# Kernel optimization log

Measured on AMD Instinct MI355X. Metric: run time of the kernel, lower is better.

## Reference

```python
import jax, jax.numpy as jnp
import numpy as np

SPATIAL_SHAPES = ((100, 167), (50, 84), (25, 42), (13, 21))
NUM_HEADS = 8
NUM_LEVELS = 4
NUM_POINTS = 4
EMBED_DIM = 256
LV = sum(h * w for h, w in SPATIAL_SHAPES)  # 22223


def bilinear_sample(img, grid):
    """torch.F.grid_sample(mode='bilinear', padding_mode='zeros', align_corners=False).
    img: (B, D, H, W); grid: (B, Lq, P, 2) with xy in [-1, 1]. Returns (B, D, Lq, P)."""
    B, D, H, W = img.shape
    x = (grid[..., 0] + 1.0) * 0.5 * W - 0.5  # (B, Lq, P)
    y = (grid[..., 1] + 1.0) * 0.5 * H - 0.5
    x0 = jnp.floor(x)
    y0 = jnp.floor(y)
    wx1 = x - x0
    wy1 = y - y0
    wx0 = 1.0 - wx1
    wy0 = 1.0 - wy1

    def gather(ix, iy):
        valid = ((ix >= 0) & (ix <= W - 1) & (iy >= 0) & (iy <= H - 1)).astype(img.dtype)
        ixc = jnp.clip(ix, 0, W - 1).astype(jnp.int32)
        iyc = jnp.clip(iy, 0, H - 1).astype(jnp.int32)

        def g(img_b, ixb, iyb, vb):
            return img_b[:, iyb, ixb] * vb[None]  # (D, Lq, P)

        return jax.vmap(g)(img, ixc, iyc, valid)  # (B, D, Lq, P)

    v00 = gather(x0, y0)
    v01 = gather(x0 + 1, y0)
    v10 = gather(x0, y0 + 1)
    v11 = gather(x0 + 1, y0 + 1)
    w00 = (wy0 * wx0)[:, None]
    w01 = (wy0 * wx1)[:, None]
    w10 = (wy1 * wx0)[:, None]
    w11 = (wy1 * wx1)[:, None]
    return v00 * w00 + v01 * w01 + v10 * w10 + v11 * w11


def deform_attn(query, ref_points, value, W_off, b_off, W_attn, b_attn, W_val, b_val, W_out, b_out):
    N, Lq, C = query.shape
    D = C // NUM_HEADS
    off = (query @ W_off + b_off).reshape(N, Lq, NUM_HEADS, NUM_LEVELS, NUM_POINTS, 2)
    attn = jax.nn.softmax((query @ W_attn + b_attn).reshape(N, Lq, NUM_HEADS, NUM_LEVELS * NUM_POINTS), axis=-1)
    attn = attn.reshape(N, Lq, NUM_HEADS, NUM_LEVELS, NUM_POINTS)
    ref_cxcy = ref_points[:, :, None, :, None, :2]
    ref_wh = ref_points[:, :, None, :, None, 2:]
    loc = ref_cxcy + off / NUM_POINTS * ref_wh * 0.5
    grids = 2.0 * loc - 1.0  # (N, Lq, nh, L, P, 2)

    v = value @ W_val + b_val  # (N, Lv, C)
    sampled = []
    start = 0
    for lvl, (H, W) in enumerate(SPATIAL_SHAPES):
        v_l = v[:, start:start + H * W]  # (N, HW, C)
        start += H * W
        v_l = v_l.transpose(0, 2, 1).reshape(N * NUM_HEADS, D, H, W)
        g_l = grids[:, :, :, lvl].transpose(0, 2, 1, 3, 4).reshape(N * NUM_HEADS, Lq, NUM_POINTS, 2)
        sampled.append(bilinear_sample(v_l, g_l))  # (N*nh, D, Lq, P)
    sampled = jnp.concatenate(sampled, axis=-1)  # (N*nh, D, Lq, L*P)

    attn_r = attn.transpose(0, 2, 1, 3, 4).reshape(N * NUM_HEADS, 1, Lq, NUM_LEVELS * NUM_POINTS)
    out = (sampled * attn_r).sum(-1)  # (N*nh, D, Lq)
    out = out.reshape(N, C, Lq).transpose(0, 2, 1)
    return out @ W_out + b_out


def setup_inputs() -> dict:
    key = jax.random.key(0)
    ks = jax.random.split(key, 8)
    N, Lq, C = 1, LV, EMBED_DIM
    s = 0.02
    return {
        "query": jax.random.normal(ks[0], (N, Lq, C), jnp.float32),
        "ref_points": jax.random.uniform(ks[1], (N, Lq, NUM_LEVELS, 4), jnp.float32),
        "value": jax.random.normal(ks[2], (N, LV, C), jnp.float32),
        "W_off": jax.random.normal(ks[3], (C, NUM_HEADS * NUM_LEVELS * NUM_POINTS * 2), jnp.float32) * s,
        "b_off": jnp.zeros((NUM_HEADS * NUM_LEVELS * NUM_POINTS * 2,), jnp.float32),
        "W_attn": jax.random.normal(ks[4], (C, NUM_HEADS * NUM_LEVELS * NUM_POINTS), jnp.float32) * s,
        "b_attn": jnp.zeros((NUM_HEADS * NUM_LEVELS * NUM_POINTS,), jnp.float32),
        "W_val": jax.random.normal(ks[5], (C, C), jnp.float32) * s,
        "b_val": jnp.zeros((C,), jnp.float32),
        "W_out": jax.random.normal(ks[6], (C, C), jnp.float32) * s,
        "b_out": jnp.zeros((C,), jnp.float32),
    }


def reference(query, ref_points, value, W_off, b_off, W_attn, b_attn, W_val, b_val, W_out, b_out):
    return deform_attn(query, ref_points, value, W_off, b_off, W_attn, b_attn, W_val, b_val, W_out, b_out)
```

## Files before the change

kernel.cpp:

```cpp
#include <hip/hip_runtime.h>
#include <math.h>

#define LQ 22223
#define NH 8
#define NL 4
#define NP 4
#define CDIM 256

typedef __attribute__((ext_vector_type(8))) short short8;
typedef __attribute__((ext_vector_type(4))) float f32x4;

__device__ __forceinline__ ushort f2bf(float f) {
    union { float f; unsigned u; } c; c.f = f;
    unsigned u = c.u;
    return (ushort)((u + 0x7fffu + ((u >> 16) & 1u)) >> 16);
}
__device__ __forceinline__ float bflo(unsigned u) {
    union { unsigned u; float f; } c; c.u = u << 16; return c.f;
}
__device__ __forceinline__ float bfhi(unsigned u) {
    union { unsigned u; float f; } c; c.u = u & 0xffff0000u; return c.f;
}

__global__ __launch_bounds__(256) void convert_act(
    const float4* __restrict__ q, const float4* __restrict__ v,
    ushort* __restrict__ qb, ushort* __restrict__ vb, int n8each)
{
    int i = blockIdx.x * 256 + threadIdx.x;
    const float4* src; ushort* dst; int j;
    if (i < n8each) { src = q; dst = qb; j = i; }
    else if (i < 2 * n8each) { src = v; dst = vb; j = i - n8each; }
    else return;
    const float4 a = src[2 * j];
    const float4 b = src[2 * j + 1];
    short8 o;
    o[0] = (short)f2bf(a.x); o[1] = (short)f2bf(a.y);
    o[2] = (short)f2bf(a.z); o[3] = (short)f2bf(a.w);
    o[4] = (short)f2bf(b.x); o[5] = (short)f2bf(b.y);
    o[6] = (short)f2bf(b.z); o[7] = (short)f2bf(b.w);
    *reinterpret_cast<short8*>(dst + 8 * j) = o;
}

__global__ __launch_bounds__(256) void convert_wt(
    const float* __restrict__ Wv, const float* __restrict__ Wo,
    const float* __restrict__ Wu, const float* __restrict__ Wa,
    const float* __restrict__ bo, const float* __restrict__ ba,
    ushort* __restrict__ Tv, ushort* __restrict__ Toa,
    ushort* __restrict__ Tu, float* __restrict__ bcat)
{
    int idx = blockIdx.x * 256 + threadIdx.x;
    if (idx >= 229376) {
        int b = idx - 229376;
        if (b < 384) bcat[b] = (b < 256) ? bo[b] : ba[b - 256];
        return;
    }
    const float* W; ushort* T; int N; int local;
    if      (idx < 65536)  { W = Wv; T = Tv;          N = 256; local = idx; }
    else if (idx < 131072) { W = Wo; T = Toa;         N = 256; local = idx - 65536; }
    else if (idx < 196608) { W = Wu; T = Tu;          N = 256; local = idx - 131072; }
    else                   { W = Wa; T = Toa + 65536; N = 128; local = idx - 196608; }
    int k = local & 255;
    int n = local >> 8;
    T[n * 256 + k] = f2bf(W[k * N + n]);
}

template <typename OutT>
__global__ __launch_bounds__(256) void gemm_bf16(
    const ushort* __restrict__ A, const ushort* __restrict__ Bt,
    const float* __restrict__ bias, OutT* __restrict__ C,
    int M, int N)
{
    const int K = 256;
    __shared__ ushort As[64 * 40];
    __shared__ ushort Bs[64 * 40];

    const int tid = threadIdx.x;
    const int w = tid >> 6;
    const int l = tid & 63;
    const int bm = blockIdx.y * 64;
    const int bn = blockIdx.x * 64;

    const int r = tid >> 2;
    const int c = tid & 3;

    const int m_l  = (w << 4) + (l & 15);
    const int koff = (l >> 4) << 3;

    f32x4 acc[4] = {};

    for (int k0 = 0; k0 < K; k0 += 32) {
        short8 av = {0, 0, 0, 0, 0, 0, 0, 0};
        if (bm + r < M)
            av = *reinterpret_cast<const short8*>(A + (size_t)(bm + r) * K + k0 + c * 8);
        const short8 bv = *reinterpret_cast<const short8*>(
            Bt + (size_t)(bn + r) * K + k0 + c * 8);

        __syncthreads();
        *reinterpret_cast<short8*>(&As[r * 40 + c * 8]) = av;
        *reinterpret_cast<short8*>(&Bs[r * 40 + c * 8]) = bv;
        __syncthreads();

        const short8 af = *reinterpret_cast<const short8*>(&As[m_l * 40 + koff]);
        #pragma unroll
        for (int t = 0; t < 4; ++t) {
            const short8 bf = *reinterpret_cast<const short8*>(
                &Bs[(t * 16 + (l & 15)) * 40 + koff]);
            acc[t] = __builtin_amdgcn_mfma_f32_16x16x32_bf16(af, bf, acc[t], 0, 0, 0);
        }
    }

    const int row0 = bm + (w << 4) + ((l >> 4) << 2);
    #pragma unroll
    for (int t = 0; t < 4; ++t) {
        const int col = bn + t * 16 + (l & 15);
        const float bs = bias[col];
        #pragma unroll
        for (int i = 0; i < 4; ++i) {
            const int row = row0 + i;
            if (row < M) {
                const float o = acc[t][i] + bs;
                if constexpr (sizeof(OutT) == 2)
                    C[(size_t)row * N + col] = (OutT)f2bf(o);
                else
                    C[(size_t)row * N + col] = (OutT)o;
            }
        }
    }
}

__global__ __launch_bounds__(256) void softmax16(float* __restrict__ offattn, int rows)
{
    const int r = blockIdx.x * 256 + threadIdx.x;
    if (r >= rows) return;
    const int q = r >> 3;
    const int h = r & 7;
    float4* p = reinterpret_cast<float4*>(offattn + (size_t)q * 384 + 256 + h * 16);
    float v[16];
    #pragma unroll
    for (int i = 0; i < 4; ++i) {
        const float4 f = p[i];
        v[i * 4 + 0] = f.x; v[i * 4 + 1] = f.y; v[i * 4 + 2] = f.z; v[i * 4 + 3] = f.w;
    }
    float m = v[0];
    #pragma unroll
    for (int i = 1; i < 16; ++i) m = fmaxf(m, v[i]);
    float s = 0.f;
    #pragma unroll
    for (int i = 0; i < 16; ++i) { v[i] = expf(v[i] - m); s += v[i]; }
    const float inv = 1.f / s;
    #pragma unroll
    for (int i = 0; i < 4; ++i)
        p[i] = make_float4(v[i * 4 + 0] * inv, v[i * 4 + 1] * inv,
                           v[i * 4 + 2] * inv, v[i * 4 + 3] * inv);
}

__global__ __launch_bounds__(256) void msda_sample(
    const ushort* __restrict__ v, const float* __restrict__ offattn,
    const float* __restrict__ ref, ushort* __restrict__ outp)
{
    __shared__ int4   s_off[1024];
    __shared__ float4 s_wts[1024];

    const int h = blockIdx.x & 7;
    const int qbase = (blockIdx.x >> 3) * 64;
    const int tid = threadIdx.x;

    const int Hs[4] = {100, 50, 25, 13};
    const int Ws[4] = {167, 84, 42, 21};
    const int starts[4] = {0, 16700, 20900, 21950};
    const int h32 = h * 32;

    #pragma unroll
    for (int t2 = 0; t2 < 4; ++t2) {
        const int t = t2 * 256 + tid;
        const int qi = t & 63;
        const int pi = t >> 6;
        const int q = qbase + qi;
        if (q < LQ) {
            const int l = pi >> 2;
            const int W = Ws[l], H = Hs[l];
            const float* refq = ref + (size_t)q * (NL * 4) + l * 4;
            const float cx = refq[0], cy = refq[1], rw = refq[2], rh = refq[3];
            const float* row = offattn + (size_t)q * 384;
            const float ox = row[h32 + pi * 2];
            const float oy = row[h32 + pi * 2 + 1];
            const float wgt = row[256 + h * 16 + pi];

            const float lx = cx + ox * 0.125f * rw;
            const float ly = cy + oy * 0.125f * rh;
            const float x = lx * (float)W - 0.5f;
            const float y = ly * (float)H - 0.5f;

            const float x0f = floorf(x);
            const float y0f = floorf(y);
            const int x0 = (int)x0f, y0 = (int)y0f;
            const float wx1 = x - x0f, wy1 = y - y0f;
            const float wx0 = 1.f - wx1, wy0 = 1.f - wy1;

            const bool xv0 = (x0 >= 0) && (x0 < W);
            const bool xv1 = (x0 + 1 >= 0) && (x0 + 1 < W);
            const bool yv0 = (y0 >= 0) && (y0 < H);
            const bool yv1 = (y0 + 1 >= 0) && (y0 + 1 < H);

            const int x0c = min(max(x0, 0), W - 1);
            const int x1c = min(max(x0 + 1, 0), W - 1);
            const int y0c = min(max(y0, 0), H - 1);
            const int y1c = min(max(y0 + 1, 0), H - 1);

            int4 ob;
            ob.x = ((starts[l] + y0c * W + x0c) << 8) + h32;
            ob.y = ((starts[l] + y0c * W + x1c) << 8) + h32;
            ob.z = ((starts[l] + y1c * W + x0c) << 8) + h32;
            ob.w = ((starts[l] + y1c * W + x1c) << 8) + h32;
            float4 wb;
            wb.x = (xv0 && yv0) ? wgt * wy0 * wx0 : 0.f;
            wb.y = (xv1 && yv0) ? wgt * wy0 * wx1 : 0.f;
            wb.z = (xv0 && yv1) ? wgt * wy1 * wx0 : 0.f;
            wb.w = (xv1 && yv1) ? wgt * wy1 * wx1 : 0.f;
            s_off[t] = ob;
            s_wts[t] = wb;
        }
    }
    __syncthreads();

    const int qi = tid >> 2;
    const int dg = tid & 3;
    const int q = qbase + qi;
    if (q >= LQ) return;
    const int d8 = dg * 8;

    float acc[8] = {};

    int4   o = s_off[qi];
    float4 w = s_wts[qi];
    uint4 a0 = *reinterpret_cast<const uint4*>(v + o.x + d8);
    uint4 a1 = *reinterpret_cast<const uint4*>(v + o.y + d8);
    uint4 a2 = *reinterpret_cast<const uint4*>(v + o.z + d8);
    uint4 a3 = *reinterpret_cast<const uint4*>(v + o.w + d8);

    #pragma unroll
    for (int p = 0; p < 16; ++p) {
        uint4 b0, b1, b2, b3; float4 wn;
        if (p < 15) {
            const int4 on = s_off[(p + 1) * 64 + qi];
            wn = s_wts[(p + 1) * 64 + qi];
            b0 = *reinterpret_cast<const uint4*>(v + on.x + d8);
            b1 = *reinterpret_cast<const uint4*>(v + on.y + d8);
            b2 = *reinterpret_cast<const uint4*>(v + on.z + d8);
            b3 = *reinterpret_cast<const uint4*>(v + on.w + d8);
        }
        const unsigned u0[4] = {a0.x, a0.y, a0.z, a0.w};
        const unsigned u1[4] = {a1.x, a1.y, a1.z, a1.w};
        const unsigned u2[4] = {a2.x, a2.y, a2.z, a2.w};
        const unsigned u3[4] = {a3.x, a3.y, a3.z, a3.w};
        #pragma unroll
        for (int j = 0; j < 4; ++j) {
            acc[2 * j]     += w.x * bflo(u0[j]) + w.y * bflo(u1[j])
                            + w.z * bflo(u2[j]) + w.w * bflo(u3[j]);
            acc[2 * j + 1] += w.x * bfhi(u0[j]) + w.y * bfhi(u1[j])
                            + w.z * bfhi(u2[j]) + w.w * bfhi(u3[j]);
        }
        a0 = b0; a1 = b1; a2 = b2; a3 = b3; w = wn;
    }

    short8 o8;
    #pragma unroll
    for (int j = 0; j < 8; ++j) o8[j] = (short)f2bf(acc[j]);
    *reinterpret_cast<short8*>(outp + (size_t)q * CDIM + h32 + d8) = o8;
}

extern "C" void kernel_launch(void* const* d_in, const int* in_sizes, int n_in,
                              void* d_out, int out_size, void* d_ws, size_t ws_size,
                              hipStream_t stream)
{
    const float* query  = (const float*)d_in[0];
    const float* ref    = (const float*)d_in[1];
    const float* value  = (const float*)d_in[2];
    const float* W_off  = (const float*)d_in[3];
    const float* b_off  = (const float*)d_in[4];
    const float* W_attn = (const float*)d_in[5];
    const float* b_attn = (const float*)d_in[6];
    const float* W_val  = (const float*)d_in[7];
    const float* b_val  = (const float*)d_in[8];
    const float* W_out  = (const float*)d_in[9];
    const float* b_out  = (const float*)d_in[10];
    float* out = (float*)d_out;

    char* p = (char*)d_ws;
    ushort* v_bf    = (ushort*)p; p += (size_t)LQ * CDIM * 2;
    float*  offattn = (float*)p;  p += (size_t)LQ * 384 * 4;
    ushort* q_bf    = (ushort*)p; p += (size_t)LQ * CDIM * 2;
    ushort* val_bf  = (ushort*)p; p += (size_t)LQ * CDIM * 2;
    ushort* Wt_val  = (ushort*)p; p += 65536 * 2;
    ushort* Wt_oa   = (ushort*)p; p += (65536 + 32768) * 2;
    ushort* Wt_out  = (ushort*)p; p += 65536 * 2;
    float*  bcat    = (float*)p;  p += 384 * 4;
    ushort* outp = q_bf;

    const int n8 = LQ * CDIM / 8;
    const int mblk = (LQ + 63) / 64;

    convert_act<<<(2 * n8 + 255) / 256, 256, 0, stream>>>(
        (const float4*)query, (const float4*)value, q_bf, val_bf, n8);
    convert_wt<<<(229376 + 384 + 255) / 256, 256, 0, stream>>>(
        W_val, W_off, W_out, W_attn, b_off, b_attn, Wt_val, Wt_oa, Wt_out, bcat);

    gemm_bf16<ushort><<<dim3(CDIM / 64, mblk), 256, 0, stream>>>(
        val_bf, Wt_val, b_val, v_bf, LQ, CDIM);
    gemm_bf16<float><<<dim3(384 / 64, mblk), 256, 0, stream>>>(
        q_bf, Wt_oa, bcat, offattn, LQ, 384);
    softmax16<<<(LQ * NH + 255) / 256, 256, 0, stream>>>(offattn, LQ * NH);
    const int qg = (LQ + 63) / 64;
    msda_sample<<<qg * 8, 256, 0, stream>>>(v_bf, offattn, ref, outp);
    gemm_bf16<float><<<dim3(CDIM / 64, mblk), 256, 0, stream>>>(
        outp, Wt_out, b_out, out, LQ, CDIM);
}
```

Measured before the change: 235.7 us.

## Fuse fp32-to-bf16 activation conversion into GEMMs and cover full N per block

Drops the separate activation conversion kernel. The GEMMs now read fp32 query/value directly and convert to bf16 while loading tiles. Each GEMM block now covers the full output width (16 or 24 MMA fragments), so every A row tile is read once instead of once per 64-column slab. The sampling kernel's manual software prefetch of the next point is also replaced by a plain loop. The trade-off is fewer, larger blocks (about 348) with more accumulators and shared memory each, which may reduce occupancy, and the GEMMs now read fp32 A at twice the bytes.

```diff
diff --git a/kernel.cpp b/kernel.cpp
--- a/kernel.cpp
+++ b/kernel.cpp
@@ -20,25 +20,6 @@
 }
 __device__ __forceinline__ float bfhi(unsigned u) {
     union { unsigned u; float f; } c; c.u = u & 0xffff0000u; return c.f;
-}
-
-__global__ __launch_bounds__(256) void convert_act(
-    const float4* __restrict__ q, const float4* __restrict__ v,
-    ushort* __restrict__ qb, ushort* __restrict__ vb, int n8each)
-{
-    int i = blockIdx.x * 256 + threadIdx.x;
-    const float4* src; ushort* dst; int j;
-    if (i < n8each) { src = q; dst = qb; j = i; }
-    else if (i < 2 * n8each) { src = v; dst = vb; j = i - n8each; }
-    else return;
-    const float4 a = src[2 * j];
-    const float4 b = src[2 * j + 1];
-    short8 o;
-    o[0] = (short)f2bf(a.x); o[1] = (short)f2bf(a.y);
-    o[2] = (short)f2bf(a.z); o[3] = (short)f2bf(a.w);
-    o[4] = (short)f2bf(b.x); o[5] = (short)f2bf(b.y);
-    o[6] = (short)f2bf(b.z); o[7] = (short)f2bf(b.w);
-    *reinterpret_cast<short8*>(dst + 8 * j) = o;
 }
 
 __global__ __launch_bounds__(256) void convert_wt(
@@ -64,21 +45,20 @@
     T[n * 256 + k] = f2bf(W[k * N + n]);
 }
 
-template <typename OutT>
-__global__ __launch_bounds__(256) void gemm_bf16(
-    const ushort* __restrict__ A, const ushort* __restrict__ Bt,
-    const float* __restrict__ bias, OutT* __restrict__ C,
-    int M, int N)
+template <int NFRAG, typename AT, typename OutT>
+__global__ __launch_bounds__(256) void gemm_full(
+    const AT* __restrict__ A, const ushort* __restrict__ Bt,
+    const float* __restrict__ bias, OutT* __restrict__ C, int M)
 {
     const int K = 256;
+    const int N = NFRAG * 16;
     __shared__ ushort As[64 * 40];
-    __shared__ ushort Bs[64 * 40];
+    __shared__ ushort Bs[NFRAG * 16 * 40];
 
     const int tid = threadIdx.x;
     const int w = tid >> 6;
     const int l = tid & 63;
-    const int bm = blockIdx.y * 64;
-    const int bn = blockIdx.x * 64;
+    const int bm = blockIdx.x * 64;
 
     const int r = tid >> 2;
     const int c = tid & 3;
@@ -86,23 +66,43 @@
     const int m_l  = (w << 4) + (l & 15);
     const int koff = (l >> 4) << 3;
 
-    f32x4 acc[4] = {};
+    f32x4 acc[NFRAG] = {};
 
     for (int k0 = 0; k0 < K; k0 += 32) {
         short8 av = {0, 0, 0, 0, 0, 0, 0, 0};
-        if (bm + r < M)
-            av = *reinterpret_cast<const short8*>(A + (size_t)(bm + r) * K + k0 + c * 8);
-        const short8 bv = *reinterpret_cast<const short8*>(
-            Bt + (size_t)(bn + r) * K + k0 + c * 8);
+        if (bm + r < M) {
+            if constexpr (sizeof(AT) == 4) {
+                const float4 f0 = *reinterpret_cast<const float4*>(
+                    A + (size_t)(bm + r) * K + k0 + c * 8);
+                const float4 f1 = *reinterpret_cast<const float4*>(
+                    A + (size_t)(bm + r) * K + k0 + c * 8 + 4);
+                av[0] = (short)f2bf(f0.x); av[1] = (short)f2bf(f0.y);
+                av[2] = (short)f2bf(f0.z); av[3] = (short)f2bf(f0.w);
+                av[4] = (short)f2bf(f1.x); av[5] = (short)f2bf(f1.y);
+                av[6] = (short)f2bf(f1.z); av[7] = (short)f2bf(f1.w);
+            } else {
+                av = *reinterpret_cast<const short8*>(
+                    A + (size_t)(bm + r) * K + k0 + c * 8);
+            }
+        }
+        short8 bv[NFRAG / 4];
+        #pragma unroll
+        for (int j = 0; j < NFRAG / 4; ++j) {
+            const int row = j * 64 + r;
+            bv[j] = *reinterpret_cast<const short8*>(
+                Bt + (size_t)row * K + k0 + c * 8);
+        }
 
         __syncthreads();
         *reinterpret_cast<short8*>(&As[r * 40 + c * 8]) = av;
-        *reinterpret_cast<short8*>(&Bs[r * 40 + c * 8]) = bv;
+        #pragma unroll
+        for (int j = 0; j < NFRAG / 4; ++j)
+            *reinterpret_cast<short8*>(&Bs[(j * 64 + r) * 40 + c * 8]) = bv[j];
         __syncthreads();
 
         const short8 af = *reinterpret_cast<const short8*>(&As[m_l * 40 + koff]);
         #pragma unroll
-        for (int t = 0; t < 4; ++t) {
+        for (int t = 0; t < NFRAG; ++t) {
             const short8 bf = *reinterpret_cast<const short8*>(
                 &Bs[(t * 16 + (l & 15)) * 40 + koff]);
             acc[t] = __builtin_amdgcn_mfma_f32_16x16x32_bf16(af, bf, acc[t], 0, 0, 0);
@@ -111,8 +111,8 @@
 
     const int row0 = bm + (w << 4) + ((l >> 4) << 2);
     #pragma unroll
-    for (int t = 0; t < 4; ++t) {
-        const int col = bn + t * 16 + (l & 15);
+    for (int t = 0; t < NFRAG; ++t) {
+        const int col = t * 16 + (l & 15);
         const float bs = bias[col];
         #pragma unroll
         for (int i = 0; i < 4; ++i) {
@@ -231,24 +231,14 @@
 
     float acc[8] = {};
 
-    int4   o = s_off[qi];
-    float4 w = s_wts[qi];
-    uint4 a0 = *reinterpret_cast<const uint4*>(v + o.x + d8);
-    uint4 a1 = *reinterpret_cast<const uint4*>(v + o.y + d8);
-    uint4 a2 = *reinterpret_cast<const uint4*>(v + o.z + d8);
-    uint4 a3 = *reinterpret_cast<const uint4*>(v + o.w + d8);
-
     #pragma unroll
     for (int p = 0; p < 16; ++p) {
-        uint4 b0, b1, b2, b3; float4 wn;
-        if (p < 15) {
-            const int4 on = s_off[(p + 1) * 64 + qi];
-            wn = s_wts[(p + 1) * 64 + qi];
-            b0 = *reinterpret_cast<const uint4*>(v + on.x + d8);
-            b1 = *reinterpret_cast<const uint4*>(v + on.y + d8);
-            b2 = *reinterpret_cast<const uint4*>(v + on.z + d8);
-            b3 = *reinterpret_cast<const uint4*>(v + on.w + d8);
-        }
+        const int4   o = s_off[p * 64 + qi];
+        const float4 w = s_wts[p * 64 + qi];
+        const uint4 a0 = *reinterpret_cast<const uint4*>(v + o.x + d8);
+        const uint4 a1 = *reinterpret_cast<const uint4*>(v + o.y + d8);
+        const uint4 a2 = *reinterpret_cast<const uint4*>(v + o.z + d8);
+        const uint4 a3 = *reinterpret_cast<const uint4*>(v + o.w + d8);
         const unsigned u0[4] = {a0.x, a0.y, a0.z, a0.w};
         const unsigned u1[4] = {a1.x, a1.y, a1.z, a1.w};
         const unsigned u2[4] = {a2.x, a2.y, a2.z, a2.w};
@@ -260,7 +250,6 @@
             acc[2 * j + 1] += w.x * bfhi(u0[j]) + w.y * bfhi(u1[j])
                             + w.z * bfhi(u2[j]) + w.w * bfhi(u3[j]);
         }
-        a0 = b0; a1 = b1; a2 = b2; a3 = b3; w = wn;
     }
 
     short8 o8;
@@ -289,29 +278,24 @@
     char* p = (char*)d_ws;
     ushort* v_bf    = (ushort*)p; p += (size_t)LQ * CDIM * 2;
     float*  offattn = (float*)p;  p += (size_t)LQ * 384 * 4;
-    ushort* q_bf    = (ushort*)p; p += (size_t)LQ * CDIM * 2;
-    ushort* val_bf  = (ushort*)p; p += (size_t)LQ * CDIM * 2;
+    ushort* outp    = (ushort*)p; p += (size_t)LQ * CDIM * 2;
     ushort* Wt_val  = (ushort*)p; p += 65536 * 2;
     ushort* Wt_oa   = (ushort*)p; p += (65536 + 32768) * 2;
     ushort* Wt_out  = (ushort*)p; p += 65536 * 2;
     float*  bcat    = (float*)p;  p += 384 * 4;
-    ushort* outp = q_bf;
-
-    const int n8 = LQ * CDIM / 8;
+
     const int mblk = (LQ + 63) / 64;
 
-    convert_act<<<(2 * n8 + 255) / 256, 256, 0, stream>>>(
-        (const float4*)query, (const float4*)value, q_bf, val_bf, n8);
     convert_wt<<<(229376 + 384 + 255) / 256, 256, 0, stream>>>(
         W_val, W_off, W_out, W_attn, b_off, b_attn, Wt_val, Wt_oa, Wt_out, bcat);
 
-    gemm_bf16<ushort><<<dim3(CDIM / 64, mblk), 256, 0, stream>>>(
-        val_bf, Wt_val, b_val, v_bf, LQ, CDIM);
-    gemm_bf16<float><<<dim3(384 / 64, mblk), 256, 0, stream>>>(
-        q_bf, Wt_oa, bcat, offattn, LQ, 384);
+    gemm_full<16, float, ushort><<<mblk, 256, 0, stream>>>(
+        value, Wt_val, b_val, v_bf, LQ);
+    gemm_full<24, float, float><<<mblk, 256, 0, stream>>>(
+        query, Wt_oa, bcat, offattn, LQ);
     softmax16<<<(LQ * NH + 255) / 256, 256, 0, stream>>>(offattn, LQ * NH);
     const int qg = (LQ + 63) / 64;
     msda_sample<<<qg * 8, 256, 0, stream>>>(v_bf, offattn, ref, outp);
-    gemm_bf16<float><<<dim3(CDIM / 64, mblk), 256, 0, stream>>>(
-        outp, Wt_out, b_out, out, LQ, CDIM);
-}
+    gemm_full<16, ushort, float><<<mblk, 256, 0, stream>>>(
+        outp, Wt_out, b_out, out, LQ);
+}
```

New measurement: 251.2 us. 6.6% more time.
